# Optimization experiments

Hardware: AMD Instinct MI355X
Metric: run time of the kernel (lower is better)

The kernel has to match this reference:

```python
import jax, jax.numpy as jnp
import numpy as np

N = 10000
E = 160000


def _lin(key, fi, fo):
    kw, kb = jax.random.split(key)
    W = jax.random.normal(kw, (fi, fo), dtype=jnp.float32) * 0.02
    b = jnp.zeros((fo,), dtype=jnp.float32)
    return W, b


def setup_inputs() -> dict:
    key = jax.random.key(0)
    ks = jax.random.split(key, 20)
    inp = {}
    inp['x'] = jax.random.normal(ks[0], (N, 2048), dtype=jnp.float32)
    src = jax.random.randint(ks[1], (E,), 0, N)
    dst = jax.random.randint(ks[2], (E,), 0, N)
    inp['edge_index'] = jnp.stack([src, dst]).astype(jnp.int64)
    dims = [(2048, 1024), (1024, 2048), (2048, 1024), (1024, 2048)]
    ki = 3
    for li, (fi, fo) in enumerate(dims, start=1):
        for name in ('q', 'k', 'v', 's'):
            W, b = _lin(ks[ki], fi, fo)
            ki += 1
            inp[f'W{li}{name}'] = W
            inp[f'b{li}{name}'] = b
    return inp


def _tconv(x, src, dst, Wq, bq, Wk, bk, Wv, bv, Ws, bs):
    # PyG TransformerConv, heads=1: per-edge attention j->i, softmax over
    # incoming edges of each target node i, plus root (skip) linear.
    q = x @ Wq + bq                      # [N, C]
    k = x @ Wk + bk
    v = x @ Wv + bv
    C = q.shape[-1]
    logits = jnp.sum(q[dst] * k[src], axis=-1) / jnp.sqrt(jnp.float32(C))  # [E]
    m = jax.ops.segment_max(logits, dst, num_segments=N)   # per-node max
    m = jnp.where(jnp.isfinite(m), m, 0.0)                  # isolated nodes
    e = jnp.exp(logits - m[dst])
    s = jax.ops.segment_sum(e, dst, num_segments=N)
    alpha = e / (s[dst] + 1e-16)                            # [E]
    agg = jax.ops.segment_sum(v[src] * alpha[:, None], dst, num_segments=N)
    return agg + x @ Ws + bs


def reference(x, edge_index,
              W1q, b1q, W1k, b1k, W1v, b1v, W1s, b1s,
              W2q, b2q, W2k, b2k, W2v, b2v, W2s, b2s,
              W3q, b3q, W3k, b3k, W3v, b3v, W3s, b3s,
              W4q, b4q, W4k, b4k, W4v, b4v, W4s, b4s):
    src, dst = edge_index[0], edge_index[1]
    h1 = jax.nn.elu(_tconv(x, src, dst, W1q, b1q, W1k, b1k, W1v, b1v, W1s, b1s))
    h2 = _tconv(h1, src, dst, W2q, b2q, W2k, b2k, W2v, b2v, W2s, b2s)
    h3 = jax.nn.elu(_tconv(h2, src, dst, W3q, b3q, W3k, b3k, W3v, b3v, W3s, b3s))
    out = _tconv(h3, src, dst, W4q, b4q, W4k, b4k, W4v, b4v, W4s, b4s)
    return out
```

## Files before the change

### kernel.cpp

```cpp
#include <hip/hip_runtime.h>
#include <cmath>
#include <cstddef>
#include <cstdint>

typedef __attribute__((ext_vector_type(8))) _Float16 half8_t;
typedef __attribute__((ext_vector_type(4))) _Float16 half4_t;
typedef __attribute__((ext_vector_type(2))) _Float16 half2_t;
typedef __attribute__((ext_vector_type(4))) float f32x4;

__device__ __forceinline__ float dot2f16(half2_t a, half2_t b, float c) {
#if __has_builtin(__builtin_amdgcn_fdot2)
  return __builtin_amdgcn_fdot2(a, b, c, false);
#else
  return c + (float)a.x * (float)b.x + (float)a.y * (float)b.y;
#endif
}

__device__ __forceinline__ void gload16(const unsigned short* g,
                                        unsigned short* l) {
  __builtin_amdgcn_global_load_lds(
      (const __attribute__((address_space(1))) unsigned int*)g,
      (__attribute__((address_space(3))) unsigned int*)l, 16, 0, 0);
}

__global__ __launch_bounds__(256) void cast_f16_k(
    const float* __restrict__ in, unsigned short* __restrict__ out, size_t n4) {
  size_t i = (size_t)blockIdx.x * blockDim.x + threadIdx.x;
  if (i >= n4) return;
  float4 v = ((const float4*)in)[i];
  half4_t h;
  h.x = (_Float16)v.x;
  h.y = (_Float16)v.y;
  h.z = (_Float16)v.z;
  h.w = (_Float16)v.w;
  ((half4_t*)out)[i] = h;
}

__global__ __launch_bounds__(256) void transp_f16_k(
    const float* __restrict__ W0, const float* __restrict__ W1,
    const float* __restrict__ W2, const float* __restrict__ W3,
    unsigned short* __restrict__ T, int K, int C) {
  __shared__ float t[32][33];
  const int m = blockIdx.z;
  const float* W = (m == 0) ? W0 : (m == 1) ? W1 : (m == 2) ? W2 : W3;
  _Float16* th = (_Float16*)T + (size_t)m * C * K;
  int k0 = blockIdx.x * 32, c0 = blockIdx.y * 32;
  int tx = threadIdx.x & 31, ty = threadIdx.x >> 5;
#pragma unroll
  for (int r = 0; r < 4; ++r)
    t[ty + r * 8][tx] = W[(size_t)(k0 + ty + r * 8) * C + c0 + tx];
  __syncthreads();
#pragma unroll
  for (int r = 0; r < 4; ++r) {
    int c = ty + r * 8;
    th[(size_t)(c0 + c) * K + k0 + tx] = (_Float16)t[tx][c];
  }
}

__global__ __launch_bounds__(256) void gemm_f16_k(
    const unsigned short* __restrict__ Ab, const unsigned short* __restrict__ Wt,
    const float* __restrict__ bq, const float* __restrict__ bk,
    const float* __restrict__ bv, const float* __restrict__ bs,
    unsigned short* __restrict__ Qh, unsigned short* __restrict__ Kh,
    unsigned short* __restrict__ Vh, float* __restrict__ S, int M, int K,
    int C, int NX, int NY) {
  __shared__ unsigned short lds[2][2][4096];

  const int nwg = NX * NY;
  const int bid = blockIdx.x;
  const int qq = nwg >> 3, rr = nwg & 7;
  const int xcd = bid & 7, idx = bid >> 3;
  const int wgid =
      (xcd < rr ? xcd * (qq + 1) : rr * (qq + 1) + (xcd - rr) * qq) + idx;
  const int by = wgid % NY, bx = wgid / NY;

  const int bm = bx * 128, n0 = by * 128;
  const int kind = n0 / C;
  const int tid = threadIdx.x;
  const int lane = tid & 63, w = tid >> 6;
  const int wm = w >> 1, wn = w & 1;
  const int fr = lane & 15, kg = lane >> 4;

  const int srow = w * 32 + (lane >> 2);
  const int soff = (lane & 3) * 8;
  const size_t ga0 = (size_t)min(bm + srow, M - 1) * K + soff;
  const size_t ga1 = (size_t)min(bm + srow + 16, M - 1) * K + soff;
  const size_t gb0 = (size_t)(n0 + srow) * K + soff;
  const size_t gb1 = (size_t)(n0 + srow + 16) * K + soff;
  const int l0 = w * 1024, l1 = w * 1024 + 512;

  f32x4 acc[4][4];
#pragma unroll
  for (int i = 0; i < 4; ++i)
#pragma unroll
    for (int j = 0; j < 4; ++j) acc[i][j] = (f32x4)0.f;

  gload16(Ab + ga0, &lds[0][0][l0]);
  gload16(Ab + ga1, &lds[0][0][l1]);
  gload16(Wt + gb0, &lds[0][1][l0]);
  gload16(Wt + gb1, &lds[0][1][l1]);
  __syncthreads();

  const int T = K / 32;
  for (int t = 0; t < T; ++t) {
    const int cur = t & 1;
    if (t + 1 < T) {
      const int ko = (t + 1) * 32;
      gload16(Ab + ga0 + ko, &lds[cur ^ 1][0][l0]);
      gload16(Ab + ga1 + ko, &lds[cur ^ 1][0][l1]);
      gload16(Wt + gb0 + ko, &lds[cur ^ 1][1][l0]);
      gload16(Wt + gb1 + ko, &lds[cur ^ 1][1][l1]);
    }
    const unsigned short* As = lds[cur][0];
    const unsigned short* Bs = lds[cur][1];
    half8_t ah[4], bh[4];
#pragma unroll
    for (int i = 0; i < 4; ++i) {
      ah[i] = *(const half8_t*)(As + (wm * 64 + i * 16 + fr) * 32 + kg * 8);
      bh[i] = *(const half8_t*)(Bs + (wn * 64 + i * 16 + fr) * 32 + kg * 8);
    }
#pragma unroll
    for (int i = 0; i < 4; ++i)
#pragma unroll
      for (int j = 0; j < 4; ++j)
        acc[i][j] = __builtin_amdgcn_mfma_f32_16x16x32_f16(ah[i], bh[j],
                                                           acc[i][j], 0, 0, 0);
    __syncthreads();
  }

  const float* bptr = (kind == 0) ? bq : (kind == 1) ? bk : (kind == 2) ? bv : bs;
  const int cbase = (n0 - kind * C) + wn * 64;
  float bvv[4];
#pragma unroll
  for (int j = 0; j < 4; ++j) bvv[j] = bptr[cbase + j * 16 + fr];

  unsigned short* obu = (kind == 0) ? Qh : (kind == 1) ? Kh : Vh;
  _Float16* ob = (_Float16*)obu;
#pragma unroll
  for (int i = 0; i < 4; ++i) {
#pragma unroll
    for (int r = 0; r < 4; ++r) {
      int gr = bm + wm * 64 + i * 16 + kg * 4 + r;
      if (gr < M) {
        if (kind == 3) {
#pragma unroll
          for (int j = 0; j < 4; ++j)
            S[(size_t)gr * C + cbase + j * 16 + fr] = acc[i][j][r] + bvv[j];
        } else {
#pragma unroll
          for (int j = 0; j < 4; ++j)
            ob[(size_t)gr * C + cbase + j * 16 + fr] =
                (_Float16)(acc[i][j][r] + bvv[j]);
        }
      }
    }
  }
}

__global__ __launch_bounds__(256) void attn_fused2_k(
    const unsigned short* __restrict__ Qh, const unsigned short* __restrict__ Kh,
    const unsigned short* __restrict__ Vh, const int* __restrict__ rowptr,
    const int* __restrict__ csr_src, float* __restrict__ gscratch,
    float* __restrict__ skipio, unsigned short* __restrict__ Hb, int C,
    float scale, int do_elu, int writeH) {
  __shared__ _Float16 qs[2048];
  __shared__ float ebuf[512];
  __shared__ int ssrc[512];
  __shared__ float wred[8];
  const int i = blockIdx.x;
  const int tid = threadIdx.x;
  const int lane = tid & 63, wid = tid >> 6;
  const int beg = rowptr[i], end = rowptr[i + 1];
  const int deg = end - beg;
  const bool sm = (deg <= 512);

  for (int c0 = tid * 4; c0 < C; c0 += 1024)
    *(uint2*)&qs[c0] = *(const uint2*)(Qh + (size_t)i * C + c0);
  if (sm)
    for (int p = tid; p < deg; p += 256) ssrc[p] = csr_src[beg + p];
  if (tid < 8) wred[tid] = (tid < 4) ? -INFINITY : 0.f;
  __syncthreads();

  if (deg > 0) {
    float wmaxv = -INFINITY;
    for (int ep = wid; ep < deg; ep += 4) {
      int s = sm ? ssrc[ep] : csr_src[beg + ep];
      const unsigned short* kr = Kh + (size_t)s * C;
      float sum = 0.f;
      for (int c0 = lane * 8; c0 < C; c0 += 512) {
        uint4 kk = *(const uint4*)(kr + c0);
        uint4 qq4 = *(const uint4*)&qs[c0];
        const half2_t* kp = (const half2_t*)&kk;
        const half2_t* qp = (const half2_t*)&qq4;
        sum = dot2f16(kp[0], qp[0], sum);
        sum = dot2f16(kp[1], qp[1], sum);
        sum = dot2f16(kp[2], qp[2], sum);
        sum = dot2f16(kp[3], qp[3], sum);
      }
#pragma unroll
      for (int o = 32; o; o >>= 1) sum += __shfl_xor(sum, o);
      float lg = sum * scale;
      if (lane == 0) {
        if (sm) ebuf[ep] = lg; else gscratch[beg + ep] = lg;
      }
      wmaxv = fmaxf(wmaxv, lg);
    }
    if (lane == 0) wred[wid] = wmaxv;
    __syncthreads();
    float m = fmaxf(fmaxf(wred[0], wred[1]), fmaxf(wred[2], wred[3]));

    float part = 0.f;
    for (int ep = tid; ep < deg; ep += 256) {
      float lg = sm ? ebuf[ep] : gscratch[beg + ep];
      float e = expf(lg - m);
      if (sm) ebuf[ep] = e; else gscratch[beg + ep] = e;
      part += e;
    }
#pragma unroll
    for (int o = 32; o; o >>= 1) part += __shfl_xor(part, o);
    if (lane == 0) wred[4 + wid] = part;
  }
  __syncthreads();

  float total = wred[4] + wred[5] + wred[6] + wred[7];
  float denom = 1.f / (total + 1e-16f);
  const int cpt = C >> 8;
  const int col0 = tid * cpt;
  float acc[8];
#pragma unroll
  for (int j = 0; j < 8; ++j) acc[j] = 0.f;

  for (int ep = 0; ep < deg; ++ep) {
    float a = (sm ? ebuf[ep] : gscratch[beg + ep]) * denom;
    int s = sm ? ssrc[ep] : csr_src[beg + ep];
    const unsigned short* vr = Vh + (size_t)s * C + col0;
    if (cpt == 4) {
      ushort4 pv = *(const ushort4*)vr;
      const _Float16* ph = (const _Float16*)&pv;
#pragma unroll
      for (int u = 0; u < 4; ++u) acc[u] = fmaf(a, (float)ph[u], acc[u]);
    } else {
      uint4 pv = *(const uint4*)vr;
      const _Float16* ph = (const _Float16*)&pv;
#pragma unroll
      for (int u = 0; u < 8; ++u) acc[u] = fmaf(a, (float)ph[u], acc[u]);
    }
  }

  float* srow = skipio + (size_t)i * C + col0;
#pragma unroll
  for (int v4 = 0; v4 < 2; ++v4) {
    if (v4 * 4 < cpt) {
      float4 o = *(const float4*)(srow + v4 * 4);
      o.x += acc[v4 * 4 + 0];
      o.y += acc[v4 * 4 + 1];
      o.z += acc[v4 * 4 + 2];
      o.w += acc[v4 * 4 + 3];
      if (do_elu) {
        o.x = o.x > 0.f ? o.x : expm1f(o.x);
        o.y = o.y > 0.f ? o.y : expm1f(o.y);
        o.z = o.z > 0.f ? o.z : expm1f(o.z);
        o.w = o.w > 0.f ? o.w : expm1f(o.w);
      }
      if (writeH) {
        half4_t h;
        h.x = (_Float16)o.x;
        h.y = (_Float16)o.y;
        h.z = (_Float16)o.z;
        h.w = (_Float16)o.w;
        *(half4_t*)((_Float16*)Hb + (size_t)i * C + col0 + v4 * 4) = h;
      } else {
        *(float4*)(srow + v4 * 4) = o;
      }
    }
  }
}

__global__ void count_deg_k(const int* __restrict__ dst, int E,
                            int* __restrict__ cnt) {
  int e = blockIdx.x * blockDim.x + threadIdx.x;
  if (e < E) atomicAdd(&cnt[dst[e]], 1);
}

__global__ void scan_k(const int* __restrict__ cnt, int* __restrict__ rowptr,
                       int N) {
  __shared__ int part[1024];
  int t = threadIdx.x;
  int per = (N + 1023) >> 10;
  int base = t * per;
  int s = 0;
  for (int i = 0; i < per; ++i) {
    int idx = base + i;
    if (idx < N) s += cnt[idx];
  }
  part[t] = s;
  __syncthreads();
  for (int off = 1; off < 1024; off <<= 1) {
    int v = (t >= off) ? part[t - off] : 0;
    __syncthreads();
    part[t] += v;
    __syncthreads();
  }
  int run = part[t] - s;
  for (int i = 0; i < per; ++i) {
    int idx = base + i;
    if (idx < N) {
      rowptr[idx] = run;
      run += cnt[idx];
    }
  }
  if (t == 1023) rowptr[N] = part[1023];
}

__global__ void scatter_csr_k(const int* __restrict__ src,
                              const int* __restrict__ dst, int E,
                              const int* __restrict__ rowptr,
                              int* __restrict__ fill,
                              int* __restrict__ csr_src) {
  int e = blockIdx.x * blockDim.x + threadIdx.x;
  if (e >= E) return;
  int d = dst[e];
  int pos = rowptr[d] + atomicAdd(&fill[d], 1);
  csr_src[pos] = src[e];
}

extern "C" void kernel_launch(void* const* d_in, const int* in_sizes, int n_in,
                              void* d_out, int out_size, void* d_ws,
                              size_t ws_size, hipStream_t stream) {
  const float* x = (const float*)d_in[0];
  const int* eidx = (const int*)d_in[1];
  const int N = in_sizes[0] / 2048;
  const int E = in_sizes[1] / 2;
  const int* srcA = eidx;
  const int* dstA = eidx + E;
  float* dout = (float*)d_out;

  char* p = (char*)d_ws;
  auto alloc = [&](size_t bytes) {
    void* r = (void*)p;
    p += (bytes + 255) & ~(size_t)255;
    return r;
  };

  float* logits = (float*)alloc((size_t)E * 4);
  int* rowptr = (int*)alloc((size_t)(N + 1) * 4);
  int* cnt = (int*)alloc((size_t)N * 4);
  int* fill = (int*)alloc((size_t)N * 4);
  int* csr_src = (int*)alloc((size_t)E * 4);

  hipMemsetAsync(cnt, 0, (size_t)N * 4, stream);
  hipMemsetAsync(fill, 0, (size_t)N * 4, stream);
  count_deg_k<<<(E + 255) / 256, 256, 0, stream>>>(dstA, E, cnt);
  scan_k<<<1, 1024, 0, stream>>>(cnt, rowptr, N);
  scatter_csr_k<<<(E + 255) / 256, 256, 0, stream>>>(srcA, dstA, E, rowptr,
                                                     fill, csr_src);

  const size_t szH = (size_t)N * 2048 * 2;
  const size_t szWt = (size_t)4 * 1024 * 2048 * 2;

  unsigned short* Hb = (unsigned short*)alloc(szH);
  unsigned short* Qh = (unsigned short*)alloc(szH);
  unsigned short* Kh = (unsigned short*)alloc(szH);
  unsigned short* Vh = (unsigned short*)alloc(szH);
  unsigned short* Wt = (unsigned short*)alloc(szWt);

  const int fi[4] = {2048, 1024, 2048, 1024};
  const int fo[4] = {1024, 2048, 1024, 2048};
  const int elu[4] = {1, 0, 1, 0};

  cast_f16_k<<<(int)(((size_t)N * 2048 / 4 + 255) / 256), 256, 0, stream>>>(
      x, Hb, (size_t)N * 2048 / 4);

  for (int L = 0; L < 4; ++L) {
    const int K = fi[L], C = fo[L];
    const int b = 2 + L * 8;
    const float scale = (float)(1.0 / sqrt((double)C));
    transp_f16_k<<<dim3(K / 32, C / 32, 4), 256, 0, stream>>>(
        (const float*)d_in[b + 0], (const float*)d_in[b + 2],
        (const float*)d_in[b + 4], (const float*)d_in[b + 6], Wt, K, C);
    const int NX = (N + 127) / 128;
    const int NY = 4 * C / 128;
    gemm_f16_k<<<NX * NY, 256, 0, stream>>>(
        Hb, Wt, (const float*)d_in[b + 1], (const float*)d_in[b + 3],
        (const float*)d_in[b + 5], (const float*)d_in[b + 7], Qh, Kh, Vh, dout,
        N, K, C, NX, NY);
    attn_fused2_k<<<N, 256, 0, stream>>>(Qh, Kh, Vh, rowptr, csr_src, logits,
                                         dout, Hb, C, scale, elu[L],
                                         L < 3 ? 1 : 0);
  }
}
```

Before: 1.676 ms.

## Triple-buffer GEMM LDS staging with explicit vmcnt waits and single barrier

Moves the f16 MFMA GEMM from a double-buffered LDS pipeline to a three-stage ring. Loads run two K-tiles ahead, and each iteration waits with an explicit s_waitcnt vmcnt and one s_barrier instead of two __syncthreads. The aim is to hide global-to-LDS load latency and cut barrier stalls per K step. It raises LDS use per block, which may lower occupancy, and it depends on hand-counted vmcnt values matching the four loads issued per stage.

```diff
diff --git a/kernel.cpp b/kernel.cpp
--- a/kernel.cpp
+++ b/kernel.cpp
@@ -64,7 +64,7 @@
     unsigned short* __restrict__ Qh, unsigned short* __restrict__ Kh,
     unsigned short* __restrict__ Vh, float* __restrict__ S, int M, int K,
     int C, int NX, int NY) {
-  __shared__ unsigned short lds[2][2][4096];
+  __shared__ unsigned short lds[3][2][4096];
 
   const int nwg = NX * NY;
   const int bid = blockIdx.x;
@@ -95,24 +95,32 @@
 #pragma unroll
     for (int j = 0; j < 4; ++j) acc[i][j] = (f32x4)0.f;
 
-  gload16(Ab + ga0, &lds[0][0][l0]);
-  gload16(Ab + ga1, &lds[0][0][l1]);
-  gload16(Wt + gb0, &lds[0][1][l0]);
-  gload16(Wt + gb1, &lds[0][1][l1]);
-  __syncthreads();
+  auto STAGE = [&](int buf, int ko) {
+    gload16(Ab + ga0 + ko, &lds[buf][0][l0]);
+    gload16(Ab + ga1 + ko, &lds[buf][0][l1]);
+    gload16(Wt + gb0 + ko, &lds[buf][1][l0]);
+    gload16(Wt + gb1 + ko, &lds[buf][1][l1]);
+  };
 
   const int T = K / 32;
+  STAGE(0, 0);
+  STAGE(1, 32);
+
+  int buf = 0;
   for (int t = 0; t < T; ++t) {
-    const int cur = t & 1;
-    if (t + 1 < T) {
-      const int ko = (t + 1) * 32;
-      gload16(Ab + ga0 + ko, &lds[cur ^ 1][0][l0]);
-      gload16(Ab + ga1 + ko, &lds[cur ^ 1][0][l1]);
-      gload16(Wt + gb0 + ko, &lds[cur ^ 1][1][l0]);
-      gload16(Wt + gb1 + ko, &lds[cur ^ 1][1][l1]);
-    }
-    const unsigned short* As = lds[cur][0];
-    const unsigned short* Bs = lds[cur][1];
+    if (t + 1 < T)
+      asm volatile("s_waitcnt vmcnt(4)" ::: "memory");
+    else
+      asm volatile("s_waitcnt vmcnt(0)" ::: "memory");
+    __builtin_amdgcn_s_barrier();
+    asm volatile("" ::: "memory");
+    if (t + 2 < T) {
+      int nb = buf + 2;
+      if (nb >= 3) nb -= 3;
+      STAGE(nb, (t + 2) * 32);
+    }
+    const unsigned short* As = lds[buf][0];
+    const unsigned short* Bs = lds[buf][1];
     half8_t ah[4], bh[4];
 #pragma unroll
     for (int i = 0; i < 4; ++i) {
@@ -125,7 +133,8 @@
       for (int j = 0; j < 4; ++j)
         acc[i][j] = __builtin_amdgcn_mfma_f32_16x16x32_f16(ah[i], bh[j],
                                                            acc[i][j], 0, 0, 0);
-    __syncthreads();
+    asm volatile("s_waitcnt lgkmcnt(0)" ::: "memory");
+    buf = (buf == 2) ? 0 : buf + 1;
   }
 
   const float* bptr = (kind == 0) ? bq : (kind == 1) ? bk : (kind == 2) ? bv : bs;
```

After: 1.654 ms. Within noise of the previous version (-1.3%).
